# Performance work log

Measured on AMD Instinct MI355X. Metric: run time of the kernel, lower is better.

Reference implementation:

```python
import math
import jax, jax.numpy as jnp
import numpy as np

B, L, D_MODEL, NHEAD, FACTOR = 8, 4096, 1024, 16, 5
D_HEAD = D_MODEL // NHEAD
SAMPLE_K = min(L, max(1, FACTOR * int(math.ceil(math.log(max(L, 2))))))  # 45
TOP_U = min(L, max(1, FACTOR * int(math.ceil(math.log(max(L, 2))))))     # 45


def setup_inputs() -> dict:
    key = jax.random.key(0)
    ks = jax.random.split(key, 10)
    x = jax.random.normal(ks[0], (B, L, D_MODEL), dtype=jnp.float32)
    sample_idx = jax.random.randint(ks[1], (SAMPLE_K,), 0, L)
    s = 0.02
    Wq = jax.random.normal(ks[2], (D_MODEL, D_MODEL), dtype=jnp.float32) * s
    Wk = jax.random.normal(ks[3], (D_MODEL, D_MODEL), dtype=jnp.float32) * s
    Wv = jax.random.normal(ks[4], (D_MODEL, D_MODEL), dtype=jnp.float32) * s
    Wo = jax.random.normal(ks[5], (D_MODEL, D_MODEL), dtype=jnp.float32) * s
    bq = jnp.zeros((D_MODEL,), dtype=jnp.float32)
    bk = jnp.zeros((D_MODEL,), dtype=jnp.float32)
    bv = jnp.zeros((D_MODEL,), dtype=jnp.float32)
    bo = jnp.zeros((D_MODEL,), dtype=jnp.float32)
    return {"x": x, "Wq": Wq, "bq": bq, "Wk": Wk, "bk": bk, "Wv": Wv, "bv": bv, "Wo": Wo, "bo": bo, "sample_idx": sample_idx}


def _split_heads(t):
    b, l, _ = t.shape
    return t.reshape(b, l, NHEAD, D_HEAD).transpose(0, 2, 1, 3)  # (b, h, l, d)


def reference(x, Wq, bq, Wk, bk, Wv, bv, Wo, bo, sample_idx):
    b, l, d = x.shape
    q = _split_heads(x @ Wq.T + bq)  # (b, h, l, dh)
    k = _split_heads(x @ Wk.T + bk)
    v = _split_heads(x @ Wv.T + bv)
    scale = 1.0 / math.sqrt(D_HEAD)

    # sparsity measurement on sampled keys
    k_sample = k[:, :, sample_idx, :]                          # (b, h, S, dh)
    scores_sample = jnp.einsum('bhqd,bhsd->bhqs', q, k_sample) * scale
    m = scores_sample.max(axis=-1) - scores_sample.mean(axis=-1)  # (b, h, l)
    _, top_idx = jax.lax.top_k(m, TOP_U)                       # (b, h, U)

    # mean-of-values initialization for non-selected queries
    context = jnp.broadcast_to(v.mean(axis=-2, keepdims=True), (b, NHEAD, l, D_HEAD))

    # dense attention only for the top-U queries
    q_top = jnp.take_along_axis(q, top_idx[..., None], axis=2)  # (b, h, U, dh)
    scores_top = jnp.einsum('bhud,bhkd->bhuk', q_top, k) * scale
    attn = jax.nn.softmax(scores_top, axis=-1)
    out_top = jnp.einsum('bhuk,bhkd->bhud', attn, v)            # (b, h, U, dh)

    bi = jnp.arange(b)[:, None, None]
    hi = jnp.arange(NHEAD)[None, :, None]
    context = context.at[bi, hi, top_idx].set(out_top)          # scatter back

    out = context.transpose(0, 2, 1, 3).reshape(b, l, d)
    return out @ Wo.T + bo
```

## Files before the change

### kernel.cpp

```cpp
#include <hip/hip_runtime.h>
#include <cfloat>
#include <cstdint>

#define B_  8
#define L_  4096
#define DM  1024
#define NH  16
#define DH  64
#define SK  45

typedef __attribute__((ext_vector_type(4))) float f32x4;
typedef _Float16 f16;
typedef __attribute__((ext_vector_type(4))) _Float16 f16x4;
typedef __attribute__((ext_vector_type(8))) _Float16 f16x8;

__device__ __forceinline__ void gload_lds16(const void* g, void* l) {
  __builtin_amdgcn_global_load_lds(
      (const __attribute__((address_space(1))) unsigned int*)g,
      (__attribute__((address_space(3))) unsigned int*)l, 16, 0, 0);
}

__device__ __forceinline__ int swz(int row, int c) {
  return row * 32 + (c ^ (((row >> 1) & 3) << 3));
}

__global__ __launch_bounds__(256) void xsplit16_kernel(const float* __restrict__ x,
    f16* __restrict__ xh, int n4) {
  int i = blockIdx.x * 256 + threadIdx.x;
  int stride = gridDim.x * 256;
  for (; i < n4; i += stride) {
    f32x4 v = ((const f32x4*)x)[i];
    f16x4 h;
    #pragma unroll
    for (int j = 0; j < 4; ++j) h[j] = (f16)v[j];
    ((f16x4*)xh)[i] = h;
  }
}

__global__ __launch_bounds__(256) void wsplit16_kernel(const float* __restrict__ w,
    f16* __restrict__ wh, f16* __restrict__ wl, int n4, int withlo) {
  int i = blockIdx.x * 256 + threadIdx.x;
  int stride = gridDim.x * 256;
  for (; i < n4; i += stride) {
    f32x4 v = ((const f32x4*)w)[i];
    f16x4 h, l;
    #pragma unroll
    for (int j = 0; j < 4; ++j) {
      h[j] = (f16)v[j];
      l[j] = (f16)((v[j] - (float)h[j]) * 2048.0f);
    }
    ((f16x4*)wh)[i] = h;
    if (withlo) ((f16x4*)wl)[i] = l;
  }
}

__global__ __launch_bounds__(256) void meansum_kernel(const f16* __restrict__ xh,
                                                      float* __restrict__ meanx) {
  int b = blockIdx.x;
  int d = blockIdx.y * 256 + threadIdx.x;
  int l0 = blockIdx.z * 256;
  const f16* p = xh + ((size_t)b * L_ + l0) * DM + d;
  float s = 0.f;
  for (int i = 0; i < 256; ++i) s += (float)p[(size_t)i * DM];
  atomicAdd(&meanx[b * DM + d], s);
}

__global__ __launch_bounds__(256) void meansum32_kernel(const float* __restrict__ x,
                                                        float* __restrict__ meanx) {
  int b = blockIdx.x;
  int d = blockIdx.y * 256 + threadIdx.x;
  int l0 = blockIdx.z * 256;
  const float* p = x + ((size_t)b * L_ + l0) * DM + d;
  float s = 0.f;
  for (int i = 0; i < 256; ++i) s += p[(size_t)i * DM];
  atomicAdd(&meanx[b * DM + d], s);
}

__global__ __launch_bounds__(256) void proj_vec_kernel(const float* __restrict__ vin,
    const float* __restrict__ W, const float* __restrict__ bias,
    float* __restrict__ vout, float scale) {
  int g = blockIdx.x * 256 + threadIdx.x;
  int b = g >> 10, n = g & 1023;
  const float* xr = vin + b * DM;
  const float* wr = W + (size_t)n * DM;
  float a0 = 0, a1 = 0, a2 = 0, a3 = 0;
  for (int d = 0; d < DM; d += 4) {
    a0 += xr[d + 0] * wr[d + 0];
    a1 += xr[d + 1] * wr[d + 1];
    a2 += xr[d + 2] * wr[d + 2];
    a3 += xr[d + 3] * wr[d + 3];
  }
  vout[g] = ((a0 + a1) + (a2 + a3)) * scale + bias[n];
}

__global__ __launch_bounds__(256, 4) void ksample_kernel(const float* __restrict__ x,
    const float* __restrict__ Wk, const float* __restrict__ bk,
    const int* __restrict__ sidx, float* __restrict__ KS) {
  const int b = blockIdx.x, nc = blockIdx.y, sg = blockIdx.z;
  __shared__ float xs[5][32];
  __shared__ float wk[64][33];
  __shared__ float red[4][5][64];
  __shared__ int ls[5];
  const int tid = threadIdx.x;
  const int nl = tid & 63, kq = tid >> 6;
  if (tid < 5) ls[tid] = sidx[sg * 5 + tid];
  float acc[5] = {0.f, 0.f, 0.f, 0.f, 0.f};
  const int wrow = tid >> 2, wq = tid & 3;
  for (int kt = 0; kt < 32; ++kt) {
    const int d0 = kt * 32;
    __syncthreads();
    if (tid < 40) {
      int s = tid >> 3, q = tid & 7;
      *(f32x4*)&xs[s][q * 4] = *(const f32x4*)&x[((size_t)b * L_ + ls[s]) * DM + d0 + q * 4];
    }
    {
      const float* src = &Wk[(size_t)(nc * 64 + wrow) * DM + d0 + wq * 8];
      *(f32x4*)&wk[wrow][wq * 8]     = *(const f32x4*)src;
      *(f32x4*)&wk[wrow][wq * 8 + 4] = *(const f32x4*)(src + 4);
    }
    __syncthreads();
    #pragma unroll
    for (int i = 0; i < 2; ++i) {
      f32x4 w = *(const f32x4*)&wk[nl][kq * 8 + i * 4];
      #pragma unroll
      for (int s = 0; s < 5; ++s) {
        f32x4 xv = *(const f32x4*)&xs[s][kq * 8 + i * 4];
        acc[s] += xv[0] * w[0] + xv[1] * w[1] + xv[2] * w[2] + xv[3] * w[3];
      }
    }
  }
  #pragma unroll
  for (int s = 0; s < 5; ++s) red[kq][s][nl] = acc[s];
  __syncthreads();
  for (int t = tid; t < 5 * 64; t += 256) {
    int s = t >> 6, j = t & 63;
    int nj = nc * 64 + j;
    KS[((size_t)b * SK + sg * 5 + s) * DM + nj] =
        red[0][s][j] + red[1][s][j] + red[2][s][j] + red[3][s][j] + bk[nj];
  }
}

__global__ __launch_bounds__(256, 4) void pcomp_kernel(const float* __restrict__ Wq,
    const float* __restrict__ KS, f16* __restrict__ PH, f16* __restrict__ PL) {
  const int b = blockIdx.x, h = blockIdx.y, nc = blockIdx.z;
  __shared__ float ks[45][64];
  __shared__ float wqT[64][68];
  const int tid = threadIdx.x;
  const int n0 = nc * 64;
  for (int i = tid; i < 45 * 64; i += 256) {
    int s = i >> 6, d = i & 63;
    ks[s][d] = KS[((size_t)b * SK + s) * DM + h * 64 + d];
  }
  for (int t = tid; t < 1024; t += 256) {
    int row = t >> 4, cg = t & 15;
    f32x4 v = *(const f32x4*)&Wq[(size_t)(h * 64 + row) * DM + n0 + cg * 4];
    #pragma unroll
    for (int j = 0; j < 4; ++j) wqT[cg * 4 + j][row] = v[j];
  }
  __syncthreads();
  for (int t = tid; t < 48 * 64; t += 256) {
    int s = t >> 6, c = t & 63;
    float acc = 0.f;
    if (s < SK) {
      const f32x4* wr = (const f32x4*)&wqT[c][0];
      const f32x4* kr = (const f32x4*)&ks[s][0];
      float a0 = 0, a1 = 0, a2 = 0, a3 = 0;
      #pragma unroll
      for (int i = 0; i < 16; ++i) {
        f32x4 wv = wr[i], kv = kr[i];
        a0 += wv[0] * kv[0]; a1 += wv[1] * kv[1];
        a2 += wv[2] * kv[2]; a3 += wv[3] * kv[3];
      }
      acc = (a0 + a1) + (a2 + a3);
    }
    f16 hv = (f16)acc;
    size_t off = ((size_t)b * 768 + h * 48 + s) * DM + n0 + c;
    PH[off] = hv;
    PL[off] = (f16)((acc - (float)hv) * 2048.0f);
  }
}

__global__ __launch_bounds__(256, 2) void gemm_sc(const float* __restrict__ x,
    const f16* __restrict__ PH, const f16* __restrict__ PL,
    float* __restrict__ SC) {
  __shared__ f16 xh[128 * 32];
  __shared__ f16 xl[128 * 32];
  __shared__ f16 wh[128 * 32];
  __shared__ f16 wl[128 * 32];
  const int tid = threadIdx.x;
  const int g = blockIdx.y * 8 + blockIdx.x;
  const int q = g >> 3;
  const int nt = q % 6;
  const int mt = (g & 7) + (q / 6) * 8;
  const int n0 = nt * 128;
  const int m0 = mt * 128;
  const int bb = mt >> 5;
  const int lane = tid & 63;
  const int wave = tid >> 6;
  const int wr = (wave >> 1) * 64;
  const int wc = (wave & 1) * 64;
  const int frow = lane & 15;
  const int fk = (lane >> 4) * 8;

  f32x4 aH[4][4], aL[4][4];
  #pragma unroll
  for (int i = 0; i < 4; ++i)
    #pragma unroll
    for (int j = 0; j < 4; ++j)
      #pragma unroll
      for (int z = 0; z < 4; ++z) { aH[i][j][z] = 0.f; aL[i][j][z] = 0.f; }

  const int ar = tid >> 1;
  const int ac = (tid & 1) * 16;
  const int r2 = tid >> 2;
  const int cb = (tid & 3) * 8;
  const int cbs = cb ^ (((r2 >> 1) & 3) << 3);

  const size_t pbase = (size_t)bb * 768;
  for (int kt = 0; kt < 32; ++kt) {
    const float* gx = x + (size_t)(m0 + ar) * DM + kt * 32 + ac;
    #pragma unroll
    for (int gi = 0; gi < 4; ++gi) {
      f32x4 v = ((const f32x4*)gx)[gi];
      f16x4 h, l;
      #pragma unroll
      for (int z = 0; z < 4; ++z) {
        h[z] = (f16)v[z];
        l[z] = (f16)((v[z] - (float)h[z]) * 2048.0f);
      }
      *(f16x4*)(xh + swz(ar, ac + gi * 4)) = h;
      *(f16x4*)(xl + swz(ar, ac + gi * 4)) = l;
    }
    gload_lds16(PH + (pbase + n0 + r2) * DM + kt * 32 + cbs,      wh + r2 * 32 + cb);
    gload_lds16(PH + (pbase + n0 + r2 + 64) * DM + kt * 32 + cbs, wh + (r2 + 64) * 32 + cb);
    gload_lds16(PL + (pbase + n0 + r2) * DM + kt * 32 + cbs,      wl + r2 * 32 + cb);
    gload_lds16(PL + (pbase + n0 + r2 + 64) * DM + kt * 32 + cbs, wl + (r2 + 64) * 32 + cb);
    __syncthreads();
    f16x8 ah[4], al[4], bh[4], bl[4];
    #pragma unroll
    for (int mi = 0; mi < 4; ++mi) {
      ah[mi] = *(const f16x8*)(xh + swz(wr + mi * 16 + frow, fk));
      al[mi] = *(const f16x8*)(xl + swz(wr + mi * 16 + frow, fk));
    }
    #pragma unroll
    for (int ni = 0; ni < 4; ++ni) {
      bh[ni] = *(const f16x8*)(wh + swz(wc + ni * 16 + frow, fk));
      bl[ni] = *(const f16x8*)(wl + swz(wc + ni * 16 + frow, fk));
    }
    #pragma unroll
    for (int mi = 0; mi < 4; ++mi)
      #pragma unroll
      for (int ni = 0; ni < 4; ++ni) {
        aH[mi][ni] = __builtin_amdgcn_mfma_f32_16x16x32_f16(ah[mi], bh[ni], aH[mi][ni], 0, 0, 0);
        aL[mi][ni] = __builtin_amdgcn_mfma_f32_16x16x32_f16(ah[mi], bl[ni], aL[mi][ni], 0, 0, 0);
        aL[mi][ni] = __builtin_amdgcn_mfma_f32_16x16x32_f16(al[mi], bh[ni], aL[mi][ni], 0, 0, 0);
      }
    __syncthreads();
  }

  #pragma unroll
  for (int mi = 0; mi < 4; ++mi) {
    int rowb = m0 + wr + mi * 16 + (lane >> 4) * 4;
    #pragma unroll
    for (int ni = 0; ni < 4; ++ni) {
      int col = n0 + wc + ni * 16 + (lane & 15);
      #pragma unroll
      for (int j = 0; j < 4; ++j) {
        SC[(size_t)(rowb + j) * 768 + col] =
            (aH[mi][ni][j] + aL[mi][ni][j] * (1.0f / 2048.0f)) * 0.125f;
      }
    }
  }
}

__global__ __launch_bounds__(256) void mcompute_kernel(const float* __restrict__ SC,
    float* __restrict__ Mout) {
  const int b = blockIdx.x;
  const int l = blockIdx.y * 16 + (threadIdx.x >> 4);
  const int h = threadIdx.x & 15;
  const float* p = SC + ((size_t)(b * L_ + l)) * 768 + h * 48;
  float mx = -FLT_MAX, sum = 0.f;
  #pragma unroll
  for (int i = 0; i < 11; ++i) {
    f32x4 v = *(const f32x4*)(p + i * 4);
    #pragma unroll
    for (int j = 0; j < 4; ++j) { mx = fmaxf(mx, v[j]); sum += v[j]; }
  }
  { float v = p[44]; mx = fmaxf(mx, v); sum += v; }
  Mout[((size_t)(b * NH + h)) * L_ + l] = mx - sum * (1.0f / SK);
}

__global__ __launch_bounds__(256) void topk_kernel(const float* __restrict__ M,
                                                   int* __restrict__ topi) {
  __shared__ float vals[L_];
  __shared__ float wv[4];
  __shared__ int wi[4];
  const int bh = blockIdx.x, tid = threadIdx.x;
  for (int i = tid; i < L_; i += 256) vals[i] = M[(size_t)bh * L_ + i];
  __syncthreads();
  const int lane = tid & 63, wave = tid >> 6;
  for (int it = 0; it < SK; ++it) {
    float best = -FLT_MAX;
    int bi = 1 << 30;
    for (int i = tid; i < L_; i += 256) {
      float v = vals[i];
      if (v > best || (v == best && i < bi)) { best = v; bi = i; }
    }
    #pragma unroll
    for (int off = 32; off; off >>= 1) {
      float ov = __shfl_down(best, off);
      int oi = __shfl_down(bi, off);
      if (ov > best || (ov == best && oi < bi)) { best = ov; bi = oi; }
    }
    if (lane == 0) { wv[wave] = best; wi[wave] = bi; }
    __syncthreads();
    if (tid == 0) {
      float bb = wv[0]; int bj = wi[0];
      for (int w = 1; w < 4; ++w)
        if (wv[w] > bb || (wv[w] == bb && wi[w] < bj)) { bb = wv[w]; bj = wi[w]; }
      topi[bh * SK + it] = bj;
      vals[bj] = -FLT_MAX;
    }
    __syncthreads();
  }
}

__global__ __launch_bounds__(256, 4) void qtop5_kernel(const float* __restrict__ x,
    const float* __restrict__ Wq, const float* __restrict__ bq,
    const int* __restrict__ topi, f16* __restrict__ QT) {
  const int b = blockIdx.x, h = blockIdx.y, sg = blockIdx.z;
  const int bh = b * NH + h;
  __shared__ float xs[5][32];
  __shared__ float wq[64][33];
  __shared__ float red[4][5][64];
  __shared__ int ls[5];
  const int tid = threadIdx.x;
  const int nl = tid & 63, kq = tid >> 6;
  if (tid < 5) ls[tid] = topi[bh * SK + sg * 5 + tid];
  float acc[5] = {0.f, 0.f, 0.f, 0.f, 0.f};
  const int wrow = tid >> 2, wqc = tid & 3;
  for (int kt = 0; kt < 32; ++kt) {
    const int d0 = kt * 32;
    __syncthreads();
    if (tid < 40) {
      int s = tid >> 3, q = tid & 7;
      *(f32x4*)&xs[s][q * 4] = *(const f32x4*)&x[((size_t)b * L_ + ls[s]) * DM + d0 + q * 4];
    }
    {
      const float* src = &Wq[(size_t)(h * 64 + wrow) * DM + d0 + wqc * 8];
      *(f32x4*)&wq[wrow][wqc * 8]     = *(const f32x4*)src;
      *(f32x4*)&wq[wrow][wqc * 8 + 4] = *(const f32x4*)(src + 4);
    }
    __syncthreads();
    #pragma unroll
    for (int i = 0; i < 2; ++i) {
      f32x4 w = *(const f32x4*)&wq[nl][kq * 8 + i * 4];
      #pragma unroll
      for (int s = 0; s < 5; ++s) {
        f32x4 xv = *(const f32x4*)&xs[s][kq * 8 + i * 4];
        acc[s] += xv[0] * w[0] + xv[1] * w[1] + xv[2] * w[2] + xv[3] * w[3];
      }
    }
  }
  #pragma unroll
  for (int s = 0; s < 5; ++s) red[kq][s][nl] = acc[s];
  __syncthreads();
  for (int t = tid; t < 5 * 64; t += 256) {
    int s = t >> 6, j = t & 63;
    QT[bh * 3072 + (sg * 5 + s) * 64 + j] =
        (f16)(red[0][s][j] + red[1][s][j] + red[2][s][j] + red[3][s][j] + bq[h * 64 + j]);
  }
}

__global__ __launch_bounds__(256, 2) void kscore_kernel(const f16* __restrict__ XH,
    const f16* __restrict__ WKH, const f16* __restrict__ WVH,
    const float* __restrict__ bk, const float* __restrict__ bvec,
    const f16* __restrict__ QT, f16* __restrict__ S, f16* __restrict__ Vg) {
  __shared__ __align__(16) char smem[68352];
  f16* qs = (f16*)smem;
  f16* xh = (f16*)(smem + 6912);
  f16* wh = (f16*)(smem + 23296);
  f16* Kt = (f16*)(smem + 31488);
  f16* Vt = Kt;
  const int g = blockIdx.y * 128 + blockIdx.x;
  const int b = g & 7;
  const int p = g >> 3;
  const int jc = p >> 4;
  const int h = p & 15;
  const int bh = b * 16 + h;
  const int tid = threadIdx.x;
  const int lane = tid & 63, wave = tid >> 6;
  const int frow = lane & 15;
  const int fk = (lane >> 4) * 8;

  for (int i = tid; i < 48 * 64; i += 256)
    qs[(i >> 6) * 72 + (i & 63)] = QT[bh * 3072 + i];

  f32x4 accK[4][4], accV[4][4];
  #pragma unroll
  for (int i = 0; i < 4; ++i)
    #pragma unroll
    for (int j = 0; j < 4; ++j)
      #pragma unroll
      for (int z = 0; z < 4; ++z) { accK[i][j][z] = 0.f; accV[i][j][z] = 0.f; }

  const int r2 = tid >> 2, cb = (tid & 3) * 8;
  const int cbs = cb ^ (((r2 >> 1) & 3) << 3);
  for (int kt = 0; kt < 32; ++kt) {
    #pragma unroll
    for (int i = 0; i < 4; ++i)
      gload_lds16(XH + (size_t)(b * L_ + jc * 256 + i * 64 + r2) * DM + kt * 32 + cbs,
                  xh + (i * 64 + r2) * 32 + cb);
    gload_lds16(WKH + (size_t)(h * 64 + r2) * DM + kt * 32 + cbs, wh + r2 * 32 + cb);
    gload_lds16(WVH + (size_t)(h * 64 + r2) * DM + kt * 32 + cbs, wh + (r2 + 64) * 32 + cb);
    __syncthreads();
    f16x8 am[4], bnK[4], bnV[4];
    #pragma unroll
    for (int mi = 0; mi < 4; ++mi)
      am[mi] = *(const f16x8*)(xh + swz(wave * 64 + mi * 16 + frow, fk));
    #pragma unroll
    for (int ni = 0; ni < 4; ++ni) {
      bnK[ni] = *(const f16x8*)(wh + swz(ni * 16 + frow, fk));
      bnV[ni] = *(const f16x8*)(wh + swz(64 + ni * 16 + frow, fk));
    }
    #pragma unroll
    for (int mi = 0; mi < 4; ++mi)
      #pragma unroll
      for (int ni = 0; ni < 4; ++ni) {
        accK[mi][ni] = __builtin_amdgcn_mfma_f32_16x16x32_f16(am[mi], bnK[ni], accK[mi][ni], 0, 0, 0);
        accV[mi][ni] = __builtin_amdgcn_mfma_f32_16x16x32_f16(am[mi], bnV[ni], accV[mi][ni], 0, 0, 0);
      }
    __syncthreads();
  }

  #pragma unroll
  for (int mi = 0; mi < 4; ++mi) {
    int jl = wave * 64 + mi * 16 + (lane >> 4) * 4;
    #pragma unroll
    for (int ni = 0; ni < 4; ++ni) {
      int d = ni * 16 + (lane & 15);
      float bc = bk[h * 64 + d];
      #pragma unroll
      for (int z = 0; z < 4; ++z)
        Kt[(jl + z) * 72 + d] = (f16)(accK[mi][ni][z] + bc);
    }
  }
  __syncthreads();

  f32x4 accS[3][4];
  #pragma unroll
  for (int i = 0; i < 3; ++i)
    #pragma unroll
    for (int j = 0; j < 4; ++j)
      #pragma unroll
      for (int z = 0; z < 4; ++z) accS[i][j][z] = 0.f;
  #pragma unroll
  for (int ks = 0; ks < 2; ++ks) {
    f16x8 aq[3], bv[4];
    #pragma unroll
    for (int mu = 0; mu < 3; ++mu)
      aq[mu] = *(const f16x8*)(qs + (mu * 16 + frow) * 72 + ks * 32 + fk);
    #pragma unroll
    for (int nj = 0; nj < 4; ++nj)
      bv[nj] = *(const f16x8*)(Kt + (wave * 64 + nj * 16 + frow) * 72 + ks * 32 + fk);
    #pragma unroll
    for (int mu = 0; mu < 3; ++mu)
      #pragma unroll
      for (int nj = 0; nj < 4; ++nj)
        accS[mu][nj] = __builtin_amdgcn_mfma_f32_16x16x32_f16(aq[mu], bv[nj], accS[mu][nj], 0, 0, 0);
  }
  __syncthreads();

  #pragma unroll
  for (int mi = 0; mi < 4; ++mi) {
    int jl = wave * 64 + mi * 16 + (lane >> 4) * 4;
    #pragma unroll
    for (int ni = 0; ni < 4; ++ni) {
      int d = ni * 16 + (lane & 15);
      float bc = bvec[h * 64 + d];
      #pragma unroll
      for (int z = 0; z < 4; ++z)
        Vt[d * 264 + jl + z] = (f16)(accV[mi][ni][z] + bc);
    }
  }
  __syncthreads();

  for (int t = tid; t < 64 * 32; t += 256) {
    int d = t >> 5, j8 = t & 31;
    f16x8 v = *(const f16x8*)(Vt + d * 264 + j8 * 8);
    *(f16x8*)(Vg + ((size_t)bh * 64 + d) * L_ + jc * 256 + j8 * 8) = v;
  }

  #pragma unroll
  for (int mu = 0; mu < 3; ++mu) {
    #pragma unroll
    for (int nj = 0; nj < 4; ++nj) {
      int j = jc * 256 + wave * 64 + nj * 16 + (lane & 15);
      #pragma unroll
      for (int z = 0; z < 4; ++z) {
        int u = mu * 16 + (lane >> 4) * 4 + z;
        if (u < SK)
          S[((size_t)bh * SK + u) * L_ + j] = (f16)(accS[mu][nj][z] * 0.125f);
      }
    }
  }
}

__global__ __launch_bounds__(256, 2) void pv_kernel(const f16* __restrict__ S,
    const f16* __restrict__ Vg, float* __restrict__ OT, float* __restrict__ Zb) {
  __shared__ float red[4 * 48 * 64];
  const int g = blockIdx.y * 128 + blockIdx.x;
  const int b = g & 7;
  const int p = g >> 3;
  const int jc = p >> 4;
  const int h = p & 15;
  const int bh = b * 16 + h;
  const int tid = threadIdx.x;
  const int lane = tid & 63, wave = tid >> 6;
  const int frow = lane & 15;
  const int fk = (lane >> 4) * 8;

  f32x4 accO[3][4];
  float zacc[3] = {0.f, 0.f, 0.f};
  #pragma unroll
  for (int i = 0; i < 3; ++i)
    #pragma unroll
    for (int j = 0; j < 4; ++j)
      #pragma unroll
      for (int z = 0; z < 4; ++z) accO[i][j][z] = 0.f;

  #pragma unroll
  for (int ks = 0; ks < 2; ++ks) {
    f16x8 ap[3], bv[4];
    #pragma unroll
    for (int mu = 0; mu < 3; ++mu) {
      int urow = mu * 16 + frow;
      int ur = (urow < SK) ? urow : 0;
      const f16* aptr = S + ((size_t)bh * SK + ur) * L_ + jc * 256 + wave * 64 + ks * 32 + fk;
      f16x8 raw = *(const f16x8*)aptr;
      f16x8 pp;
      float zs = 0.f;
      #pragma unroll
      for (int j = 0; j < 8; ++j) {
        f16 e = (f16)__expf((float)raw[j]);
        pp[j] = e;
        zs += (float)e;
      }
      zacc[mu] += zs;
      ap[mu] = pp;
    }
    #pragma unroll
    for (int nd = 0; nd < 4; ++nd)
      bv[nd] = *(const f16x8*)(Vg + ((size_t)bh * 64 + nd * 16 + frow) * L_ +
                               jc * 256 + wave * 64 + ks * 32 + fk);
    #pragma unroll
    for (int mu = 0; mu < 3; ++mu)
      #pragma unroll
      for (int nd = 0; nd < 4; ++nd)
        accO[mu][nd] = __builtin_amdgcn_mfma_f32_16x16x32_f16(ap[mu], bv[nd], accO[mu][nd], 0, 0, 0);
  }

  #pragma unroll
  for (int mu = 0; mu < 3; ++mu) {
    float z = zacc[mu];
    z += __shfl_xor(z, 16);
    z += __shfl_xor(z, 32);
    int u = mu * 16 + frow;
    if ((lane >> 4) == 0 && u < SK) atomicAdd(&Zb[bh * 48 + u], z);
  }

  #pragma unroll
  for (int mu = 0; mu < 3; ++mu) {
    #pragma unroll
    for (int nd = 0; nd < 4; ++nd) {
      int d = nd * 16 + (lane & 15);
      #pragma unroll
      for (int z = 0; z < 4; ++z) {
        int u = mu * 16 + (lane >> 4) * 4 + z;
        red[wave * 3072 + u * 64 + d] = accO[mu][nd][z];
      }
    }
  }
  __syncthreads();
  for (int i = tid; i < 3072; i += 256) {
    int u = i >> 6;
    if (u < SK)
      atomicAdd(&OT[((size_t)bh * SK + u) * DH + (i & 63)],
                red[i] + red[3072 + i] + red[6144 + i] + red[9216 + i]);
  }
}

__global__ __launch_bounds__(256) void basewrite_kernel(const float* __restrict__ base,
                                                        float* __restrict__ out) {
  size_t i = (size_t)blockIdx.x * 256 + threadIdx.x;
  const size_t stride = (size_t)gridDim.x * 256;
  const size_t total = (size_t)B_ * L_ * (DM / 4);
  for (; i < total; i += stride) {
    size_t b = i >> 20;
    size_t c = i & 255;
    ((f32x4*)out)[i] = ((const f32x4*)base)[b * 256 + c];
  }
}

__global__ __launch_bounds__(256, 2) void corr_kernel(const float* __restrict__ OT,
    const float* __restrict__ Zb, const float* __restrict__ MV,
    const float* __restrict__ Wo, const int* __restrict__ topi,
    float* __restrict__ out) {
  __shared__ float dv[SK][64];
  __shared__ float wo[64][65];
  __shared__ float invz[SK];
  __shared__ int lidx[SK];
  const int bh = blockIdx.x, q = blockIdx.y, tid = threadIdx.x;
  const int b = bh >> 4, h = bh & 15;
  if (tid < SK) {
    invz[tid] = 1.0f / Zb[bh * 48 + tid];
    lidx[tid] = topi[bh * SK + tid];
  }
  __syncthreads();
  for (int i = tid; i < SK * 64; i += 256) {
    int u = i >> 6, d = i & 63;
    dv[u][d] = OT[((size_t)bh * SK + u) * DH + d] * invz[u] - MV[b * DM + h * DH + d];
  }
  const int nn = tid & 63, ug = tid >> 6;
  for (int c = 0; c < 4; ++c) {
    const int n0 = q * 256 + c * 64;
    __syncthreads();
    for (int t = tid; t < 1024; t += 256) {
      int row = t >> 4, vc = t & 15;
      f32x4 v = *(const f32x4*)&Wo[(size_t)(n0 + row) * DM + h * DH + vc * 4];
      *(f32x4*)&wo[row][vc * 4] = v;
    }
    __syncthreads();
    #pragma unroll
    for (int i = 0; i < 12; ++i) {
      int u = ug + i * 4;
      if (u >= SK) break;
      float a0 = 0, a1 = 0, a2 = 0, a3 = 0;
      #pragma unroll
      for (int d4 = 0; d4 < 16; ++d4) {
        f32x4 w = *(const f32x4*)&wo[nn][d4 * 4];
        f32x4 dd = *(const f32x4*)&dv[u][d4 * 4];
        a0 += dd[0] * w[0]; a1 += dd[1] * w[1];
        a2 += dd[2] * w[2]; a3 += dd[3] * w[3];
      }
      atomicAdd(&out[((size_t)b * L_ + lidx[u]) * DM + n0 + nn], (a0 + a1) + (a2 + a3));
    }
  }
}

static const size_t OFF_XH   = 0;
static const size_t OFF_WQH  = OFF_XH + 67108864;
static const size_t OFF_WQL  = OFF_WQH + 2097152;
static const size_t OFF_WKH  = OFF_WQL + 2097152;
static const size_t OFF_WVH  = OFF_WKH + 2097152;
static const size_t OFF_KS   = OFF_WVH + 2097152;
static const size_t OFF_M    = OFF_KS + 1474560;
static const size_t OFF_TOPI = OFF_M + 2097152;
static const size_t OFF_MEANX= OFF_TOPI + 23040;
static const size_t OFF_MV   = OFF_MEANX + 32768;
static const size_t OFF_BASE = OFF_MV + 32768;
static const size_t OFF_ZB   = OFF_BASE + 32768;
static const size_t OFF_QT   = OFF_ZB + 24576;
static const size_t OFF_S    = OFF_QT + 786432;
static const size_t OFF_OT   = OFF_S + 47185920;
static const size_t WS_NEED  = OFF_OT + 1474560;

extern "C" void kernel_launch(void* const* d_in, const int* in_sizes, int n_in,
                              void* d_out, int out_size, void* d_ws, size_t ws_size,
                              hipStream_t stream) {
  const float* x  = (const float*)d_in[0];
  const float* Wq = (const float*)d_in[1];
  const float* bq = (const float*)d_in[2];
  const float* Wk = (const float*)d_in[3];
  const float* bk = (const float*)d_in[4];
  const float* Wv = (const float*)d_in[5];
  const float* bv = (const float*)d_in[6];
  const float* Wo = (const float*)d_in[7];
  const float* bo = (const float*)d_in[8];
  const int* sidx = (const int*)d_in[9];
  float* out = (float*)d_out;
  char* ws = (char*)d_ws;

  if (ws_size < WS_NEED) {
    if (ws_size < 131072) return;
    float* MEANX = (float*)(ws + 0);
    float* MV    = (float*)(ws + 32768);
    float* BASE  = (float*)(ws + 65536);
    hipMemsetAsync(MEANX, 0, 32768, stream);
    meansum32_kernel<<<dim3(B_, 4, 16), 256, 0, stream>>>(x, MEANX);
    proj_vec_kernel<<<32, 256, 0, stream>>>(MEANX, Wv, bv, MV, 1.0f / L_);
    proj_vec_kernel<<<32, 256, 0, stream>>>(MV, Wo, bo, BASE, 1.0f);
    basewrite_kernel<<<2048, 256, 0, stream>>>(BASE, out);
    return;
  }

  f16*   XH   = (f16*)(ws + OFF_XH);
  f16*   WQH  = (f16*)(ws + OFF_WQH);
  f16*   WQL  = (f16*)(ws + OFF_WQL);
  f16*   WKH  = (f16*)(ws + OFF_WKH);
  f16*   WVH  = (f16*)(ws + OFF_WVH);
  float* KS   = (float*)(ws + OFF_KS);
  float* Mb   = (float*)(ws + OFF_M);
  int*   TOPI = (int*)(ws + OFF_TOPI);
  float* MEANX= (float*)(ws + OFF_MEANX);
  float* MV   = (float*)(ws + OFF_MV);
  float* BASE = (float*)(ws + OFF_BASE);
  float* ZB   = (float*)(ws + OFF_ZB);
  f16*   QT   = (f16*)(ws + OFF_QT);
  f16*   PH   = (f16*)(ws + OFF_S);
  f16*   PL   = (f16*)(ws + OFF_S + 12582912);
  f16*   Sb   = (f16*)(ws + OFF_S);
  float* OT   = (float*)(ws + OFF_OT);
  float* SC   = (float*)out;
  f16*   Vg   = (f16*)out;

  xsplit16_kernel<<<2048, 256, 0, stream>>>(x, XH, (int)((size_t)B_ * L_ * DM / 4));
  wsplit16_kernel<<<256, 256, 0, stream>>>(Wq, WQH, WQL, DM * DM / 4, 1);
  wsplit16_kernel<<<256, 256, 0, stream>>>(Wk, WKH, WKH, DM * DM / 4, 0);
  wsplit16_kernel<<<256, 256, 0, stream>>>(Wv, WVH, WVH, DM * DM / 4, 0);
  hipMemsetAsync(MEANX, 0, 32768, stream);
  hipMemsetAsync(OT, 0, 1474560, stream);
  hipMemsetAsync(ZB, 0, 24576, stream);
  hipMemsetAsync(QT, 0, 786432, stream);

  meansum_kernel<<<dim3(B_, 4, 16), 256, 0, stream>>>(XH, MEANX);
  proj_vec_kernel<<<32, 256, 0, stream>>>(MEANX, Wv, bv, MV, 1.0f / L_);
  proj_vec_kernel<<<32, 256, 0, stream>>>(MV, Wo, bo, BASE, 1.0f);

  ksample_kernel<<<dim3(B_, 16, 9), 256, 0, stream>>>(x, Wk, bk, sidx, KS);
  pcomp_kernel<<<dim3(B_, NH, 16), 256, 0, stream>>>(Wq, KS, PH, PL);
  gemm_sc<<<dim3(8, 192), 256, 0, stream>>>(x, PH, PL, SC);
  mcompute_kernel<<<dim3(B_, 256), 256, 0, stream>>>(SC, Mb);

  topk_kernel<<<B_ * NH, 256, 0, stream>>>(Mb, TOPI);
  qtop5_kernel<<<dim3(B_, NH, 9), 256, 0, stream>>>(x, Wq, bq, TOPI, QT);

  kscore_kernel<<<dim3(128, 16), 256, 0, stream>>>(XH, WKH, WVH, bk, bv, QT, Sb, Vg);
  pv_kernel<<<dim3(128, 16), 256, 0, stream>>>(Sb, Vg, OT, ZB);

  basewrite_kernel<<<2048, 256, 0, stream>>>(BASE, out);
  corr_kernel<<<dim3(B_ * NH, 4), 256, 0, stream>>>(OT, ZB, MV, Wo, TOPI, out);
}
```

Measured before the change: 854.3 us.

## Fuse PV accumulation into kscore kernel, keeping scores and V in LDS

The score kernel now exponentiates its scores in registers, writes P and V tiles to shared memory, and runs the P·V MFMA plus the normalizer atomics directly, so the separate pv_kernel is removed. This drops the global round trip of the fp16 score matrix and V (tens of MB) and one kernel launch. In exchange the fused kernel reuses the same shared memory for P, V and the reduction buffer, which adds barriers and register pressure.

```diff
diff --git a/kernel.cpp b/kernel.cpp
--- a/kernel.cpp
+++ b/kernel.cpp
@@ -375,13 +375,15 @@
 __global__ __launch_bounds__(256, 2) void kscore_kernel(const f16* __restrict__ XH,
     const f16* __restrict__ WKH, const f16* __restrict__ WVH,
     const float* __restrict__ bk, const float* __restrict__ bvec,
-    const f16* __restrict__ QT, f16* __restrict__ S, f16* __restrict__ Vg) {
+    const f16* __restrict__ QT, float* __restrict__ OT, float* __restrict__ Zb) {
   __shared__ __align__(16) char smem[68352];
   f16* qs = (f16*)smem;
   f16* xh = (f16*)(smem + 6912);
   f16* wh = (f16*)(smem + 23296);
   f16* Kt = (f16*)(smem + 31488);
-  f16* Vt = Kt;
+  f16* Ps = (f16*)smem;
+  f16* Vt = (f16*)(smem + 31488);
+  float* red = (float*)smem;
   const int g = blockIdx.y * 128 + blockIdx.x;
   const int b = g & 7;
   const int p = g >> 3;
@@ -483,91 +485,63 @@
         Vt[d * 264 + jl + z] = (f16)(accV[mi][ni][z] + bc);
     }
   }
-  __syncthreads();
-
-  for (int t = tid; t < 64 * 32; t += 256) {
-    int d = t >> 5, j8 = t & 31;
-    f16x8 v = *(const f16x8*)(Vt + d * 264 + j8 * 8);
-    *(f16x8*)(Vg + ((size_t)bh * 64 + d) * L_ + jc * 256 + j8 * 8) = v;
-  }
-
-  #pragma unroll
-  for (int mu = 0; mu < 3; ++mu) {
-    #pragma unroll
-    for (int nj = 0; nj < 4; ++nj) {
-      int j = jc * 256 + wave * 64 + nj * 16 + (lane & 15);
+  {
+    float zs[3][4];
+    #pragma unroll
+    for (int mu = 0; mu < 3; ++mu)
+      #pragma unroll
+      for (int z = 0; z < 4; ++z) zs[mu][z] = 0.f;
+    #pragma unroll
+    for (int mu = 0; mu < 3; ++mu)
+      #pragma unroll
+      for (int nj = 0; nj < 4; ++nj) {
+        int j = wave * 64 + nj * 16 + (lane & 15);
+        #pragma unroll
+        for (int z = 0; z < 4; ++z) {
+          int u = mu * 16 + (lane >> 4) * 4 + z;
+          float pv = __expf(accS[mu][nj][z] * 0.125f);
+          Ps[u * 264 + j] = (f16)pv;
+          zs[mu][z] += pv;
+        }
+      }
+    #pragma unroll
+    for (int mu = 0; mu < 3; ++mu)
       #pragma unroll
       for (int z = 0; z < 4; ++z) {
+        float v = zs[mu][z];
+        v += __shfl_xor(v, 1);
+        v += __shfl_xor(v, 2);
+        v += __shfl_xor(v, 4);
+        v += __shfl_xor(v, 8);
         int u = mu * 16 + (lane >> 4) * 4 + z;
-        if (u < SK)
-          S[((size_t)bh * SK + u) * L_ + j] = (f16)(accS[mu][nj][z] * 0.125f);
-      }
-    }
-  }
-}
-
-__global__ __launch_bounds__(256, 2) void pv_kernel(const f16* __restrict__ S,
-    const f16* __restrict__ Vg, float* __restrict__ OT, float* __restrict__ Zb) {
-  __shared__ float red[4 * 48 * 64];
-  const int g = blockIdx.y * 128 + blockIdx.x;
-  const int b = g & 7;
-  const int p = g >> 3;
-  const int jc = p >> 4;
-  const int h = p & 15;
-  const int bh = b * 16 + h;
-  const int tid = threadIdx.x;
-  const int lane = tid & 63, wave = tid >> 6;
-  const int frow = lane & 15;
-  const int fk = (lane >> 4) * 8;
+        if ((lane & 15) == 0 && u < SK) atomicAdd(&Zb[bh * 48 + u], v);
+      }
+  }
+  __syncthreads();
 
   f32x4 accO[3][4];
-  float zacc[3] = {0.f, 0.f, 0.f};
   #pragma unroll
   for (int i = 0; i < 3; ++i)
     #pragma unroll
     for (int j = 0; j < 4; ++j)
       #pragma unroll
       for (int z = 0; z < 4; ++z) accO[i][j][z] = 0.f;
-
   #pragma unroll
   for (int ks = 0; ks < 2; ++ks) {
-    f16x8 ap[3], bv[4];
-    #pragma unroll
-    for (int mu = 0; mu < 3; ++mu) {
-      int urow = mu * 16 + frow;
-      int ur = (urow < SK) ? urow : 0;
-      const f16* aptr = S + ((size_t)bh * SK + ur) * L_ + jc * 256 + wave * 64 + ks * 32 + fk;
-      f16x8 raw = *(const f16x8*)aptr;
-      f16x8 pp;
-      float zs = 0.f;
-      #pragma unroll
-      for (int j = 0; j < 8; ++j) {
-        f16 e = (f16)__expf((float)raw[j]);
-        pp[j] = e;
-        zs += (float)e;
-      }
-      zacc[mu] += zs;
-      ap[mu] = pp;
-    }
+    f16x8 ap[3], bvv[4];
+    #pragma unroll
+    for (int mu = 0; mu < 3; ++mu)
+      ap[mu] = *(const f16x8*)(Ps + (mu * 16 + frow) * 264 + wave * 64 + ks * 32 + fk);
     #pragma unroll
     for (int nd = 0; nd < 4; ++nd)
-      bv[nd] = *(const f16x8*)(Vg + ((size_t)bh * 64 + nd * 16 + frow) * L_ +
-                               jc * 256 + wave * 64 + ks * 32 + fk);
+      bvv[nd] = *(const f16x8*)(Vt + (nd * 16 + frow) * 264 + wave * 64 + ks * 32 + fk);
     #pragma unroll
     for (int mu = 0; mu < 3; ++mu)
       #pragma unroll
       for (int nd = 0; nd < 4; ++nd)
-        accO[mu][nd] = __builtin_amdgcn_mfma_f32_16x16x32_f16(ap[mu], bv[nd], accO[mu][nd], 0, 0, 0);
-  }
-
-  #pragma unroll
-  for (int mu = 0; mu < 3; ++mu) {
-    float z = zacc[mu];
-    z += __shfl_xor(z, 16);
-    z += __shfl_xor(z, 32);
-    int u = mu * 16 + frow;
-    if ((lane >> 4) == 0 && u < SK) atomicAdd(&Zb[bh * 48 + u], z);
-  }
+        accO[mu][nd] = __builtin_amdgcn_mfma_f32_16x16x32_f16(ap[mu], bvv[nd], accO[mu][nd], 0, 0, 0);
+  }
+  __syncthreads();
 
   #pragma unroll
   for (int mu = 0; mu < 3; ++mu) {
@@ -709,10 +683,8 @@
   f16*   QT   = (f16*)(ws + OFF_QT);
   f16*   PH   = (f16*)(ws + OFF_S);
   f16*   PL   = (f16*)(ws + OFF_S + 12582912);
-  f16*   Sb   = (f16*)(ws + OFF_S);
   float* OT   = (float*)(ws + OFF_OT);
   float* SC   = (float*)out;
-  f16*   Vg   = (f16*)out;
 
   xsplit16_kernel<<<2048, 256, 0, stream>>>(x, XH, (int)((size_t)B_ * L_ * DM / 4));
   wsplit16_kernel<<<256, 256, 0, stream>>>(Wq, WQH, WQL, DM * DM / 4, 1);
@@ -735,8 +707,7 @@
   topk_kernel<<<B_ * NH, 256, 0, stream>>>(Mb, TOPI);
   qtop5_kernel<<<dim3(B_, NH, 9), 256, 0, stream>>>(x, Wq, bq, TOPI, QT);
 
-  kscore_kernel<<<dim3(128, 16), 256, 0, stream>>>(XH, WKH, WVH, bk, bv, QT, Sb, Vg);
-  pv_kernel<<<dim3(128, 16), 256, 0, stream>>>(Sb, Vg, OT, ZB);
+  kscore_kernel<<<dim3(128, 16), 256, 0, stream>>>(XH, WKH, WVH, bk, bv, QT, OT, ZB);
 
   basewrite_kernel<<<2048, 256, 0, stream>>>(BASE, out);
   corr_kernel<<<dim3(B_ * NH, 4), 256, 0, stream>>>(OT, ZB, MV, Wo, TOPI, out);
```

Result: faster. 825.3 us (-3.4%).
